# Kernel tuning notes

Hardware: AMD Instinct MI355X
Metric: run time of the kernel (lower is better)

## Reference

```python
import jax, jax.numpy as jnp
import numpy as np

B, L, E, H, V, ENC = 64, 51, 512, 512, 30000, 2048


def setup_inputs() -> dict:
    key = jax.random.key(0)
    ks = jax.random.split(key, 12)
    encoder_out = jax.random.normal(ks[0], (B, ENC), jnp.float32)
    encoded_captions = jax.random.randint(ks[1], (B, L), 0, V)
    lengths = jax.random.randint(ks[2], (B,), 2, L + 1)
    lengths = lengths.at[0].set(L)  # ensure max(decode_lengths) == L-1 so T is static
    caption_lengths = lengths[:, None]

    def lin(k, out_d, in_d):
        bnd = 1.0 / np.sqrt(in_d)
        kw, kb = jax.random.split(k)
        w = jax.random.uniform(kw, (out_d, in_d), jnp.float32, -bnd, bnd)
        b = jax.random.uniform(kb, (out_d,), jnp.float32, -bnd, bnd)
        return w, b

    embedding_weight = jax.random.uniform(ks[3], (V, E), jnp.float32, -0.1, 0.1)
    w_ih, b_ih = lin(ks[4], 4 * H, E)
    w_hh, b_hh = lin(ks[5], 4 * H, H)
    w_init_h, b_init_h = lin(ks[6], H, ENC)
    w_init_c, b_init_c = lin(ks[7], H, ENC)
    w_fc = jax.random.uniform(ks[8], (V, H), jnp.float32, -0.1, 0.1)
    b_fc = jnp.zeros((V,), jnp.float32)
    return dict(encoder_out=encoder_out, encoded_captions=encoded_captions,
                caption_lengths=caption_lengths, embedding_weight=embedding_weight,
                w_ih=w_ih, b_ih=b_ih, w_hh=w_hh, b_hh=b_hh,
                w_init_h=w_init_h, b_init_h=b_init_h,
                w_init_c=w_init_c, b_init_c=b_init_c, w_fc=w_fc, b_fc=b_fc)


def _forward(encoder_out, embedding_weight, w_ih, b_ih, w_hh, b_hh,
             w_init_h, b_init_h, w_init_c, b_init_c, w_fc, b_fc,
             encoded_captions, caption_lengths):
    lengths = caption_lengths[:, 0]
    sort_ind = jnp.argsort(-lengths)          # descending-length sort
    enc = encoder_out[sort_ind]
    caps = encoded_captions[sort_ind]
    dec_len = lengths[sort_ind] - 1           # [B]
    embs = embedding_weight[caps]             # [B, L, E]
    h0 = enc @ w_init_h.T + b_init_h          # [B, H]
    c0 = enc @ w_init_c.T + b_init_c
    T = caps.shape[1] - 1                     # static max(decode_lengths)
    xs = (jnp.transpose(embs[:, :T], (1, 0, 2)), jnp.arange(T))

    # Note: the torch loop trims h,c to batch_size_t; because lengths are
    # sorted descending, trimmed rows never produce outputs again, so running
    # the full batch and masking finished rows yields identical predictions.
    def step(carry, xt):
        h, c = carry
        x, t = xt
        gates = x @ w_ih.T + b_ih + h @ w_hh.T + b_hh   # [B, 4H]
        i, f, g, o = jnp.split(gates, 4, axis=-1)       # LSTMCell gate order
        c = jax.nn.sigmoid(f) * c + jax.nn.sigmoid(i) * jnp.tanh(g)
        h = jax.nn.sigmoid(o) * jnp.tanh(c)
        preds = h @ w_fc.T + b_fc                        # dropout = identity (eval)
        preds = jnp.where((t < dec_len)[:, None], preds, 0.0)
        return (h, c), preds

    _, preds = jax.lax.scan(step, (h0, c0), xs)          # [T, B, V]
    predictions = jnp.transpose(preds, (1, 0, 2))        # [B, T, V]
    return predictions, caps, dec_len, sort_ind


def reference(encoder_out, encoded_captions, caption_lengths, embedding_weight,
              w_ih, b_ih, w_hh, b_hh, w_init_h, b_init_h, w_init_c, b_init_c,
              w_fc, b_fc):
    return _forward(encoder_out, embedding_weight, w_ih, b_ih, w_hh, b_hh,
                    w_init_h, b_init_h, w_init_c, b_init_c, w_fc, b_fc,
                    encoded_captions, caption_lengths)
```

## Files before the change

kernel.cpp:

```cpp
#include <hip/hip_runtime.h>

#define NB    64
#define LCAP  51
#define TT    50
#define HID   512
#define EMB   512
#define VOC   30000
#define ENCD  2048
#define G4    2048

typedef unsigned short u16;
typedef unsigned int   u32;
typedef __attribute__((ext_vector_type(8))) short bf16x8;
typedef __attribute__((ext_vector_type(4))) float f32x4;
typedef __attribute__((ext_vector_type(4))) unsigned int u32x4;

__device__ __forceinline__ u16 f2bf(float x) {
  union { float f; unsigned u; } v; v.f = x;
  unsigned r = v.u + 0x7fffu + ((v.u >> 16) & 1u);
  return (u16)(r >> 16);
}

__device__ __forceinline__ float fast_sigmoid(float x) {
  return 1.f / (1.f + __expf(-x));
}
__device__ __forceinline__ float fast_tanh(float x) {
  float xx = fminf(fmaxf(x, -10.f), 10.f);
  float e = __expf(2.f * xx);
  return (e - 1.f) * __frcp_rn(e + 1.f);
}

template <int SLEEP>
__device__ __forceinline__ void poll_flags16(const int* flg, int lane, u32 tt) {
  if (lane < 16) {
    const u32* myp = (const u32*)flg + lane;
    u32 f;
    for (;;) {
      asm volatile("global_load_dword %0, %1, off sc0 sc1"
                   : "=v"(f) : "v"(myp) : "memory");
      asm volatile("s_waitcnt vmcnt(0)" : "+v"(f) :: "memory");
      if (((f & 0xffu) >= tt) & (((f >> 8) & 0xffu) >= tt) &
          (((f >> 16) & 0xffu) >= tt) & ((f >> 24) >= tt)) break;
      __builtin_amdgcn_s_sleep(SLEEP);
    }
  }
}

__global__ __launch_bounds__(256) void sort_k(const int* __restrict__ cap_len,
                                              const int* __restrict__ caps,
                                              float* __restrict__ out,
                                              int* __restrict__ sind,
                                              int* __restrict__ dlen,
                                              int* __restrict__ trow,
                                              int* __restrict__ zmap,
                                              int* __restrict__ nact,
                                              int* __restrict__ flags,
                                              int* __restrict__ tileneed) {
  __shared__ int smlen[NB];
  __shared__ int smpos[NB];
  __shared__ int sdl[NB];
  __shared__ int cnt_s[TT];
  __shared__ int toff_s[TT];
  __shared__ int trow_s[NB * TT];
  int tid = threadIdx.x;
  if (tid < NB) { smlen[tid] = cap_len[tid]; flags[tid] = 0; }
  __syncthreads();
  if (tid < NB) {
    int li = smlen[tid];
    int rank = 0;
    for (int j = 0; j < NB; ++j) {
      int lj = smlen[j];
      rank += (lj > li || (lj == li && j < tid)) ? 1 : 0;
    }
    smpos[rank] = tid;
  }
  __syncthreads();
  if (tid < NB) {
    int src = smpos[tid];
    int dl = smlen[src] - 1;
    sind[tid] = src;
    dlen[tid] = dl;
    sdl[tid] = dl;
    float* caps_out = out + (size_t)NB * TT * VOC;
    for (int l = 0; l < LCAP; ++l)
      caps_out[tid * LCAP + l] = (float)caps[src * LCAP + l];
    out[96003264 + tid] = (float)dl;
    out[96003328 + tid] = (float)src;
  }
  __syncthreads();
  if (tid < TT) {
    int c = 0;
    for (int b = 0; b < NB; ++b) c += (sdl[b] > tid) ? 1 : 0;
    cnt_s[tid] = c;
  }
  __syncthreads();
  if (tid == 0) {
    int s = 0;
    for (int t = 0; t < TT; ++t) { toff_s[t] = s; s += cnt_s[t]; }
    *nact = s;
  }
  __syncthreads();
  if (tid < TT) {
    int t = tid;
    int o = toff_s[t];
    int z = t * NB - o;
    int c = cnt_s[t];
    for (int b = 0; b < NB; ++b) {
      int m = b * TT + t;
      if (b < c) trow_s[o + b] = m;
      else       zmap[z + (b - c)] = m;
    }
  }
  __syncthreads();
  int na = toff_s[TT - 1] + cnt_s[TT - 1];
  for (int k = tid; k < na; k += 256) trow[k] = trow_s[k];
  if (tid < 25) {
    int i = tid;
    if (i * 128 < na) {
      int k = min(i * 128 + 127, na - 1);
      tileneed[i] = (trow_s[k] % TT) + 2;
    }
  }
}

__global__ __launch_bounds__(256) void conv4(const float* __restrict__ src,
                                             u16* __restrict__ dst, int n4) {
  int i = blockIdx.x * 256 + threadIdx.x;
  if (i >= n4) return;
  float4 v = ((const float4*)src)[i];
  ushort4 o;
  o.x = f2bf(v.x); o.y = f2bf(v.y); o.z = f2bf(v.z); o.w = f2bf(v.w);
  ((ushort4*)dst)[i] = o;
}

__global__ __launch_bounds__(256) void conv_winit_k(const float* __restrict__ wh,
                                                    const float* __restrict__ wc,
                                                    u16* __restrict__ dst) {
  int i = blockIdx.x * 256 + threadIdx.x;
  if (i >= 524288) return;
  int e = i * 4;
  int row = e >> 11;
  int col = e & 2047;
  const float* src = (row < 512) ? (wh + (size_t)row * 2048 + col)
                                 : (wc + (size_t)(row - 512) * 2048 + col);
  float4 v = *(const float4*)src;
  ushort4 o;
  o.x = f2bf(v.x); o.y = f2bf(v.y); o.z = f2bf(v.z); o.w = f2bf(v.w);
  ((ushort4*)dst)[i] = o;
}

__global__ __launch_bounds__(256) void gather_enc_k(const float* __restrict__ enc,
                                                    const int* __restrict__ sind,
                                                    u16* __restrict__ dst) {
  int i = blockIdx.x * 256 + threadIdx.x;
  if (i >= 32768) return;
  int e = i * 4;
  int r = e >> 11;
  int k = e & 2047;
  float4 v = *(const float4*)(enc + (size_t)sind[r] * ENCD + k);
  ushort4 o;
  o.x = f2bf(v.x); o.y = f2bf(v.y); o.z = f2bf(v.z); o.w = f2bf(v.w);
  ((ushort4*)dst)[i] = o;
}

__global__ __launch_bounds__(256) void gather_x_k(const float* __restrict__ emb,
                                                  const int* __restrict__ caps,
                                                  const int* __restrict__ sind,
                                                  u16* __restrict__ dst) {
  int i = blockIdx.x * 256 + threadIdx.x;
  if (i >= 409600) return;
  int e = i * 4;
  int m = e >> 9;
  int k = e & 511;
  unsigned b = ((unsigned)m * 5243u) >> 18;
  int t = m - (int)b * TT;
  int cap = caps[sind[b] * LCAP + t];
  float4 v = *(const float4*)(emb + (size_t)cap * EMB + k);
  ushort4 o;
  o.x = f2bf(v.x); o.y = f2bf(v.y); o.z = f2bf(v.z); o.w = f2bf(v.w);
  ((ushort4*)dst)[i] = o;
}

#define BM 128
#define BN 128
#define BK 32
#define LDT 40

template <int EPI>
__global__ __launch_bounds__(256) void gemm_bt(const u16* __restrict__ A,
                                               const u16* __restrict__ Bm,
                                               int Mr, int Nr, int K,
                                               void* __restrict__ outv,
                                               float* __restrict__ out1,
                                               const float* __restrict__ bias0,
                                               const float* __restrict__ bias1) {
  __shared__ u16 As[BM * LDT];
  __shared__ u16 Bs[BN * LDT];
  int tid = threadIdx.x;
  int mBase = blockIdx.x * BM;
  int nBase = blockIdx.y * BN;

  int wid = tid >> 6, lane = tid & 63;
  int wm = (wid >> 1) * 64, wn = (wid & 1) * 64;
  int lm = lane & 15, lq = lane >> 4;

  f32x4 acc[4][4];
  for (int i = 0; i < 4; ++i)
    for (int j = 0; j < 4; ++j)
      acc[i][j] = (f32x4){0.f, 0.f, 0.f, 0.f};

  int nkt = K / BK;
  for (int kt = 0; kt < nkt; ++kt) {
    for (int it = 0; it < 2; ++it) {
      int li = tid + it * 256;
      int row = li >> 2, kq = li & 3;
      {
        int gr = min(mBase + row, Mr - 1);
        uint4 v = *(const uint4*)(A + (size_t)gr * K + kt * BK + kq * 8);
        *(uint4*)&As[row * LDT + kq * 8] = v;
      }
      {
        int gr = min(nBase + row, Nr - 1);
        uint4 v = *(const uint4*)(Bm + (size_t)gr * K + kt * BK + kq * 8);
        *(uint4*)&Bs[row * LDT + kq * 8] = v;
      }
    }
    __syncthreads();
    bf16x8 af[4], bfr[4];
    for (int i = 0; i < 4; ++i)
      af[i] = *(const bf16x8*)&As[(wm + i * 16 + lm) * LDT + lq * 8];
    for (int j = 0; j < 4; ++j)
      bfr[j] = *(const bf16x8*)&Bs[(wn + j * 16 + lm) * LDT + lq * 8];
    for (int i = 0; i < 4; ++i)
      for (int j = 0; j < 4; ++j)
        acc[i][j] = __builtin_amdgcn_mfma_f32_16x16x32_bf16(af[i], bfr[j], acc[i][j], 0, 0, 0);
    __syncthreads();
  }

  for (int i = 0; i < 4; ++i) {
    int rloc0 = wm + i * 16 + (lane >> 4) * 4;
    for (int j = 0; j < 4; ++j) {
      int col = nBase + wn + j * 16 + (lane & 15);
      for (int r = 0; r < 4; ++r) {
        int rloc = rloc0 + r;
        float v = acc[i][j][r];
        if (EPI == 0) {
          int row = mBase + rloc;
          if (row < Mr && col < Nr)
            ((float*)outv)[(size_t)row * Nr + col] = v + bias0[col] + bias1[col];
        } else {
          int row = mBase + rloc;
          if (row < Mr && col < Nr) {
            if (col < 512) {
              int jj = col >> 3;
              ((u16*)outv)[(size_t)jj * 512 + row * 8 + (col & 7)] = f2bf(v + bias0[col]);
            } else {
              out1[(size_t)row * 512 + (col - 512)] = v + bias1[col - 512];
            }
          }
        }
      }
    }
  }
}

__global__ __launch_bounds__(256, 1) void lstm_fc(const float* __restrict__ w_hh,
                                                  const float* __restrict__ xW,
                                                  const float* __restrict__ cbuf,
                                                  u32* __restrict__ hx,
                                                  u32* __restrict__ Hs32,
                                                  int* __restrict__ flg,
                                                  const u16* __restrict__ Wfc,
                                                  const float* __restrict__ b_fc,
                                                  const int* __restrict__ trow,
                                                  const int* __restrict__ zmap,
                                                  const int* __restrict__ nactp,
                                                  const int* __restrict__ tileneed,
                                                  float* __restrict__ out) {
  __shared__ __align__(16) char smem[43520];
  int tid = threadIdx.x;
  int wave = tid >> 6, lane = tid & 63;
  int lm = lane & 15, lq = lane >> 4;

  if (blockIdx.x < 64) {
    u16* wsm = (u16*)smem;
    float* gsmf = (float*)(smem + 33280);
    u32* hsh = (u32*)(smem + 33280 + 9216);
#define GSM(rr, cc) gsmf[(rr) * 36 + (cc)]
    int j = blockIdx.x;
    int u0 = j * 8;

    {
      int r = tid >> 3;
      int cc = (tid & 7) * 64;
      const float* src = w_hh + (size_t)((r >> 3) * HID + u0 + (r & 7)) * HID + cc;
      u16* dst = &wsm[r * 520 + cc];
#pragma unroll
      for (int q = 0; q < 16; ++q) {
        float4 v = ((const float4*)src)[q];
        ushort4 o; o.x = f2bf(v.x); o.y = f2bf(v.y); o.z = f2bf(v.z); o.w = f2bf(v.w);
        ((ushort4*)dst)[q] = o;
      }
    }
    __syncthreads();

    bf16x8 bfrag[2][16];
#pragma unroll
    for (int n = 0; n < 2; ++n)
#pragma unroll
      for (int kq = 0; kq < 16; ++kq)
        bfrag[n][kq] = *(const bf16x8*)&wsm[(n * 16 + lm) * 520 + kq * 32 + lq * 8];

    int b = tid >> 2, up = tid & 3;
    float creg[2];
    {
      float2 c2 = *(const float2*)&cbuf[(size_t)b * HID + u0 + 2 * up];
      creg[0] = c2.x; creg[1] = c2.y;
    }

    const int abase = lq * 256 + (wave * 16 + lm) * 4;

    for (int t = 0; t < TT; ++t) {
      const u32* hcur = hx + (size_t)(t & 1) * (NB * 256);
      u32* hnxt = hx + (size_t)((t + 1) & 1) * (NB * 256);

      float xg[4][2];
      {
        const float* xwp = xW + (size_t)(b * TT + t) * G4 + u0 + 2 * up;
#pragma unroll
        for (int g = 0; g < 4; ++g) {
          float2 v = *(const float2*)&xwp[g * HID];
          xg[g][0] = v.x; xg[g][1] = v.y;
        }
      }

      if (t > 0) {
        if (wave == 0) poll_flags16<1>(flg, lane, (u32)t);
        __syncthreads();
      }

      u32x4 raw[16];
#pragma unroll
      for (int kq = 0; kq < 16; ++kq) {
        const u32* p = hcur + abase + kq * 1024;
        asm volatile("global_load_dwordx4 %0, %1, off sc0 sc1"
                     : "=v"(raw[kq]) : "v"(p) : "memory");
      }
      asm volatile("s_waitcnt vmcnt(0)"
                   : "+v"(raw[0]), "+v"(raw[1]), "+v"(raw[2]), "+v"(raw[3]),
                     "+v"(raw[4]), "+v"(raw[5]), "+v"(raw[6]), "+v"(raw[7]),
                     "+v"(raw[8]), "+v"(raw[9]), "+v"(raw[10]), "+v"(raw[11]),
                     "+v"(raw[12]), "+v"(raw[13]), "+v"(raw[14]), "+v"(raw[15])
                   :: "memory");

      f32x4 acc0 = (f32x4){0.f, 0.f, 0.f, 0.f};
      f32x4 acc1 = (f32x4){0.f, 0.f, 0.f, 0.f};
#pragma unroll
      for (int kq = 0; kq < 16; ++kq) {
        bf16x8 a = __builtin_bit_cast(bf16x8, raw[kq]);
        acc0 = __builtin_amdgcn_mfma_f32_16x16x32_bf16(a, bfrag[0][kq], acc0, 0, 0, 0);
        acc1 = __builtin_amdgcn_mfma_f32_16x16x32_bf16(a, bfrag[1][kq], acc1, 0, 0, 0);
      }
#pragma unroll
      for (int r = 0; r < 4; ++r) {
        GSM(wave * 16 + lq * 4 + r, lm)      = acc0[r];
        GSM(wave * 16 + lq * 4 + r, 16 + lm) = acc1[r];
      }

      float hn2[2];
#pragma unroll
      for (int e = 0; e < 2; ++e) {
        int ul = 2 * up + e;
        float gi = GSM(b, ul)      + xg[0][e];
        float gf = GSM(b, 8 + ul)  + xg[1][e];
        float gg = GSM(b, 16 + ul) + xg[2][e];
        float go = GSM(b, 24 + ul) + xg[3][e];
        float cn = fast_sigmoid(gf) * creg[e] + fast_sigmoid(gi) * fast_tanh(gg);
        creg[e] = cn;
        hn2[e] = fast_sigmoid(go) * fast_tanh(cn);
      }
      hsh[b * 4 + up] = (u32)f2bf(hn2[0]) | ((u32)f2bf(hn2[1]) << 16);
      __syncthreads();

      if (tid < 64) {
        u32x4 hv = *(const u32x4*)&hsh[tid * 4];
        u32* dst = hnxt + j * 256 + tid * 4;
        asm volatile("global_store_dwordx4 %0, %1, off sc0 sc1"
                     :: "v"(dst), "v"(hv) : "memory");
        asm volatile("s_waitcnt vmcnt(0)" ::: "memory");
        if (tid == 0) {
          u32 fv = (u32)(t + 1);
          unsigned char* fj = (unsigned char*)flg + j;
          asm volatile("global_store_byte %0, %1, off sc0 sc1"
                       :: "v"(fj), "v"(fv) : "memory");
        }
        u32* hdst = Hs32 + ((size_t)tid * TT + t) * 256 + j * 4;
        asm volatile("global_store_dwordx4 %0, %1, off sc0 sc1"
                     :: "v"(hdst), "v"(hv) : "memory");
      }
    }
    if (wave == 0) {
      asm volatile("s_waitcnt vmcnt(0)" ::: "memory");
      if (lane == 0) {
        u32 fv = 51u;
        unsigned char* fj = (unsigned char*)flg + j;
        asm volatile("global_store_byte %0, %1, off sc0 sc1"
                     :: "v"(fj), "v"(fv) : "memory");
      }
    }
#undef GSM
  } else {
    u16* As = (u16*)smem;
    u16* Bs = (u16*)(smem + 10240);
    int* rmap_s = (int*)(smem + 20480);
    int* tn_s = (int*)(smem + 20992);
    const u16* HsA = (const u16*)Hs32;

    if (tid < 25) tn_s[tid] = tileneed[tid];
    int nactv = nactp[0];
    int ntiles = (nactv + 127) >> 7;
    int totjobs = ntiles * 235;
    __syncthreads();

    const int F = 192;
    int f = blockIdx.x - 64;
    int wm = (wave >> 1) * 64, wn = (wave & 1) * 64;

    int lastNeed = 0;
    for (int job = f; job < totjobs; job += F) {
      int rt = job / 235;
      int nb = job - rt * 235;
      int nBase = nb * 128;
      int need = tn_s[rt];
      if (need > lastNeed) {
        if (wave == 0) poll_flags16<64>(flg, lane, (u32)need);
        lastNeed = need;
      }
      __syncthreads();
      if (tid < 128) {
        int k = (rt << 7) + tid;
        rmap_s[tid] = trow[(k < nactv) ? k : (nactv - 1)];
      }
      __syncthreads();

      f32x4 acc[4][4];
      for (int i = 0; i < 4; ++i)
        for (int jj = 0; jj < 4; ++jj)
          acc[i][jj] = (f32x4){0.f, 0.f, 0.f, 0.f};

      for (int kt = 0; kt < 16; ++kt) {
        for (int it = 0; it < 2; ++it) {
          int li = tid + it * 256;
          int row = li >> 2, kq = li & 3;
          {
            int gr = rmap_s[row];
            uint4 v = *(const uint4*)(HsA + (size_t)gr * 512 + kt * BK + kq * 8);
            *(uint4*)&As[row * LDT + kq * 8] = v;
          }
          {
            int gb = min(nBase + row, VOC - 1);
            uint4 v = *(const uint4*)(Wfc + (size_t)gb * 512 + kt * BK + kq * 8);
            *(uint4*)&Bs[row * LDT + kq * 8] = v;
          }
        }
        __syncthreads();
        bf16x8 af[4], bfr[4];
        for (int i = 0; i < 4; ++i)
          af[i] = *(const bf16x8*)&As[(wm + i * 16 + lm) * LDT + lq * 8];
        for (int jj = 0; jj < 4; ++jj)
          bfr[jj] = *(const bf16x8*)&Bs[(wn + jj * 16 + lm) * LDT + lq * 8];
        for (int i = 0; i < 4; ++i)
          for (int jj = 0; jj < 4; ++jj)
            acc[i][jj] = __builtin_amdgcn_mfma_f32_16x16x32_bf16(af[i], bfr[jj], acc[i][jj], 0, 0, 0);
        __syncthreads();
      }

      for (int i = 0; i < 4; ++i) {
        int rloc0 = wm + i * 16 + lq * 4;
        for (int jj = 0; jj < 4; ++jj) {
          int col = nBase + wn + jj * 16 + lm;
          if (col < VOC) {
            float bias = b_fc[col];
            for (int r = 0; r < 4; ++r) {
              int m = rmap_s[rloc0 + r];
              out[(size_t)m * VOC + col] = acc[i][jj][r] + bias;
            }
          }
        }
      }
    }

    int nz = NB * TT - nactv;
    float4 zz = {0.f, 0.f, 0.f, 0.f};
    for (int r = f; r < nz; r += F) {
      float4* dst = (float4*)(out + (size_t)zmap[r] * VOC);
      for (int c4 = tid; c4 < VOC / 4; c4 += 256) dst[c4] = zz;
    }
  }
}

extern "C" void kernel_launch(void* const* d_in, const int* in_sizes, int n_in,
                              void* d_out, int out_size, void* d_ws, size_t ws_size,
                              hipStream_t stream) {
  const float* encoder_out = (const float*)d_in[0];
  const int*   caps        = (const int*)d_in[1];
  const int*   cap_len     = (const int*)d_in[2];
  const float* emb         = (const float*)d_in[3];
  const float* w_ih        = (const float*)d_in[4];
  const float* b_ih        = (const float*)d_in[5];
  const float* w_hh        = (const float*)d_in[6];
  const float* b_hh        = (const float*)d_in[7];
  const float* w_init_h    = (const float*)d_in[8];
  const float* b_init_h    = (const float*)d_in[9];
  const float* w_init_c    = (const float*)d_in[10];
  const float* b_init_c    = (const float*)d_in[11];
  const float* w_fc        = (const float*)d_in[12];
  const float* b_fc        = (const float*)d_in[13];
  float* out = (float*)d_out;

  char* ws = (char*)d_ws;
  int*   sind    = (int*)(ws + 0);
  int*   dlen    = (int*)(ws + 256);
  int*   nact    = (int*)(ws + 512);
  int*   flags   = (int*)(ws + 576);
  int*   tilend  = (int*)(ws + 640);
  int*   trow    = (int*)(ws + 832);
  int*   zmap    = (int*)(ws + 13632);
  float* cbuf    = (float*)(ws + 26496);
  u16*   hbuf    = (u16*)(ws + 157568);
  float* xW      = (float*)(ws + 288640);
  u16*   Hs      = (u16*)(ws + 26503040);
  u16*   Xb      = (u16*)(ws + 29779840);
  u16*   Wih     = (u16*)(ws + 33056640);
  u16*   Winit   = (u16*)(ws + 35153792);
  u16*   Wfc     = (u16*)(ws + 39348096);
  u16*   Ebf     = (u16*)(ws + 70068096);

  sort_k<<<1, 256, 0, stream>>>(cap_len, caps, out, sind, dlen, trow, zmap,
                                nact, flags, tilend);
  conv4<<<1024, 256, 0, stream>>>(w_ih, Wih, 262144);
  conv_winit_k<<<2048, 256, 0, stream>>>(w_init_h, w_init_c, Winit);
  conv4<<<15000, 256, 0, stream>>>(w_fc, Wfc, 3840000);
  gather_enc_k<<<128, 256, 0, stream>>>(encoder_out, sind, Ebf);
  gather_x_k<<<1600, 256, 0, stream>>>(emb, caps, sind, Xb);

  gemm_bt<1><<<dim3(1, 8), 256, 0, stream>>>(Ebf, Winit, 64, 1024, 2048,
                                             hbuf, cbuf, b_init_h, b_init_c);
  gemm_bt<0><<<dim3(25, 16), 256, 0, stream>>>(Xb, Wih, 3200, 2048, 512,
                                               xW, nullptr, b_ih, b_hh);
  lstm_fc<<<256, 256, 0, stream>>>(w_hh, xW, cbuf, (u32*)hbuf, (u32*)Hs, flags,
                                   Wfc, b_fc, trow, zmap, nact, tilend, out);
}
```

Measured before the change: 866.9 us.

## Fuse prep kernels and convert FC weights inside the persistent LSTM kernel

Merges the four small conversion and gather kernels into one prep launch to cut launch overhead. The large w_fc fp32-to-bf16 conversion moves into the FC worker blocks of the persistent LSTM kernel, so it overlaps with the recurrent blocks instead of running as a separate pass beforehand. FC jobs are now split into contiguous vocabulary-column ranges per block, so each block converts only its own columns, and are iterated row-tile-major to fit that ownership. The risks are load imbalance, more redundant loads of the A tile across columns, and reliance on each block reading only the Wfc rows it converted itself.

Result: no change. 859.8 us (-0.8%).

```diff
diff --git a/kernel.cpp b/kernel.cpp
--- a/kernel.cpp
+++ b/kernel.cpp
@@ -123,62 +123,47 @@
   }
 }
 
-__global__ __launch_bounds__(256) void conv4(const float* __restrict__ src,
-                                             u16* __restrict__ dst, int n4) {
+__global__ __launch_bounds__(256) void prep_k(const float* __restrict__ w_ih,
+                                              const float* __restrict__ wh,
+                                              const float* __restrict__ wc,
+                                              const float* __restrict__ enc,
+                                              const float* __restrict__ emb,
+                                              const int* __restrict__ caps,
+                                              const int* __restrict__ sind,
+                                              u16* __restrict__ Wih,
+                                              u16* __restrict__ Winit,
+                                              u16* __restrict__ Ebf,
+                                              u16* __restrict__ Xb) {
   int i = blockIdx.x * 256 + threadIdx.x;
-  if (i >= n4) return;
-  float4 v = ((const float4*)src)[i];
-  ushort4 o;
-  o.x = f2bf(v.x); o.y = f2bf(v.y); o.z = f2bf(v.z); o.w = f2bf(v.w);
-  ((ushort4*)dst)[i] = o;
-}
-
-__global__ __launch_bounds__(256) void conv_winit_k(const float* __restrict__ wh,
-                                                    const float* __restrict__ wc,
-                                                    u16* __restrict__ dst) {
-  int i = blockIdx.x * 256 + threadIdx.x;
-  if (i >= 524288) return;
-  int e = i * 4;
-  int row = e >> 11;
-  int col = e & 2047;
-  const float* src = (row < 512) ? (wh + (size_t)row * 2048 + col)
-                                 : (wc + (size_t)(row - 512) * 2048 + col);
+  const float* src;
+  u16* dstp;
+  if (i < 262144) {
+    src = w_ih + (size_t)i * 4;
+    dstp = Wih + (size_t)i * 4;
+  } else if (i < 786432) {
+    int e = (i - 262144) * 4;
+    int row = e >> 11, col = e & 2047;
+    src = (row < 512) ? (wh + (size_t)row * 2048 + col)
+                      : (wc + (size_t)(row - 512) * 2048 + col);
+    dstp = Winit + (size_t)(i - 262144) * 4;
+  } else if (i < 819200) {
+    int e = (i - 786432) * 4;
+    int r = e >> 11, k = e & 2047;
+    src = enc + (size_t)sind[r] * ENCD + k;
+    dstp = Ebf + (size_t)(i - 786432) * 4;
+  } else if (i < 1228800) {
+    int e = (i - 819200) * 4;
+    int m = e >> 9, k = e & 511;
+    unsigned b = ((unsigned)m * 5243u) >> 18;
+    int t = m - (int)b * TT;
+    int cap = caps[sind[b] * LCAP + t];
+    src = emb + (size_t)cap * EMB + k;
+    dstp = Xb + (size_t)(i - 819200) * 4;
+  } else return;
   float4 v = *(const float4*)src;
   ushort4 o;
   o.x = f2bf(v.x); o.y = f2bf(v.y); o.z = f2bf(v.z); o.w = f2bf(v.w);
-  ((ushort4*)dst)[i] = o;
-}
-
-__global__ __launch_bounds__(256) void gather_enc_k(const float* __restrict__ enc,
-                                                    const int* __restrict__ sind,
-                                                    u16* __restrict__ dst) {
-  int i = blockIdx.x * 256 + threadIdx.x;
-  if (i >= 32768) return;
-  int e = i * 4;
-  int r = e >> 11;
-  int k = e & 2047;
-  float4 v = *(const float4*)(enc + (size_t)sind[r] * ENCD + k);
-  ushort4 o;
-  o.x = f2bf(v.x); o.y = f2bf(v.y); o.z = f2bf(v.z); o.w = f2bf(v.w);
-  ((ushort4*)dst)[i] = o;
-}
-
-__global__ __launch_bounds__(256) void gather_x_k(const float* __restrict__ emb,
-                                                  const int* __restrict__ caps,
-                                                  const int* __restrict__ sind,
-                                                  u16* __restrict__ dst) {
-  int i = blockIdx.x * 256 + threadIdx.x;
-  if (i >= 409600) return;
-  int e = i * 4;
-  int m = e >> 9;
-  int k = e & 511;
-  unsigned b = ((unsigned)m * 5243u) >> 18;
-  int t = m - (int)b * TT;
-  int cap = caps[sind[b] * LCAP + t];
-  float4 v = *(const float4*)(emb + (size_t)cap * EMB + k);
-  ushort4 o;
-  o.x = f2bf(v.x); o.y = f2bf(v.y); o.z = f2bf(v.z); o.w = f2bf(v.w);
-  ((ushort4*)dst)[i] = o;
+  *(ushort4*)dstp = o;
 }
 
 #define BM 128
@@ -270,7 +255,8 @@
                                                   u32* __restrict__ hx,
                                                   u32* __restrict__ Hs32,
                                                   int* __restrict__ flg,
-                                                  const u16* __restrict__ Wfc,
+                                                  const float* __restrict__ w_fc,
+                                                  u16* __restrict__ Wfc,
                                                   const float* __restrict__ b_fc,
                                                   const int* __restrict__ trow,
                                                   const int* __restrict__ zmap,
@@ -424,66 +410,98 @@
 
     const int F = 192;
     int f = blockIdx.x - 64;
+    int fs = (f & 7) * 24 + (f >> 3);
+    int per = (totjobs + F - 1) / F;
+    int J0 = fs * per;
+    int J1 = min(J0 + per, totjobs);
     int wm = (wave >> 1) * 64, wn = (wave & 1) * 64;
 
-    int lastNeed = 0;
-    for (int job = f; job < totjobs; job += F) {
-      int rt = job / 235;
-      int nb = job - rt * 235;
-      int nBase = nb * 128;
-      int need = tn_s[rt];
-      if (need > lastNeed) {
-        if (wave == 0) poll_flags16<64>(flg, lane, (u32)need);
-        lastNeed = need;
+    if (J0 < J1) {
+      int p0 = J0 / ntiles, p1 = (J1 - 1) / ntiles;
+
+      for (int p = p0; p <= p1; ++p) {
+        int r0 = p * 128;
+        int r1 = min(r0 + 128, VOC);
+        int nel4 = (r1 - r0) * 128;
+        const float4* src = (const float4*)(w_fc + (size_t)r0 * 512);
+        ushort4* dst = (ushort4*)(Wfc + (size_t)r0 * 512);
+        for (int i = tid; i < nel4; i += 256) {
+          float4 v = src[i];
+          ushort4 o;
+          o.x = f2bf(v.x); o.y = f2bf(v.y); o.z = f2bf(v.z); o.w = f2bf(v.w);
+          dst[i] = o;
+        }
       }
       __syncthreads();
-      if (tid < 128) {
-        int k = (rt << 7) + tid;
-        rmap_s[tid] = trow[(k < nactv) ? k : (nactv - 1)];
-      }
-      __syncthreads();
-
-      f32x4 acc[4][4];
-      for (int i = 0; i < 4; ++i)
-        for (int jj = 0; jj < 4; ++jj)
-          acc[i][jj] = (f32x4){0.f, 0.f, 0.f, 0.f};
-
-      for (int kt = 0; kt < 16; ++kt) {
-        for (int it = 0; it < 2; ++it) {
-          int li = tid + it * 256;
-          int row = li >> 2, kq = li & 3;
-          {
-            int gr = rmap_s[row];
-            uint4 v = *(const uint4*)(HsA + (size_t)gr * 512 + kt * BK + kq * 8);
-            *(uint4*)&As[row * LDT + kq * 8] = v;
+
+      int lastNeed = 0;
+      for (int rt = 0; rt < ntiles; ++rt) {
+        int need = tn_s[rt];
+        bool any = false;
+        for (int p = p0; p <= p1; ++p) {
+          int J = p * ntiles + rt;
+          if (J >= J0 && J < J1) { any = true; break; }
+        }
+        if (!any) continue;
+        if (need > lastNeed) {
+          if (wave == 0) poll_flags16<64>(flg, lane, (u32)need);
+          lastNeed = need;
+        }
+        __syncthreads();
+        if (tid < 128) {
+          int k = (rt << 7) + tid;
+          rmap_s[tid] = trow[(k < nactv) ? k : (nactv - 1)];
+        }
+        __syncthreads();
+
+        for (int p = p0; p <= p1; ++p) {
+          int J = p * ntiles + rt;
+          if (J < J0 || J >= J1) continue;
+          int nBase = p * 128;
+
+          f32x4 acc[4][4];
+          for (int i = 0; i < 4; ++i)
+            for (int jj = 0; jj < 4; ++jj)
+              acc[i][jj] = (f32x4){0.f, 0.f, 0.f, 0.f};
+
+          for (int kt = 0; kt < 16; ++kt) {
+            for (int it = 0; it < 2; ++it) {
+              int li = tid + it * 256;
+              int row = li >> 2, kq = li & 3;
+              {
+                int gr = rmap_s[row];
+                uint4 v = *(const uint4*)(HsA + (size_t)gr * 512 + kt * BK + kq * 8);
+                *(uint4*)&As[row * LDT + kq * 8] = v;
+              }
+              {
+                int gb = min(nBase + row, VOC - 1);
+                uint4 v = *(const uint4*)(Wfc + (size_t)gb * 512 + kt * BK + kq * 8);
+                *(uint4*)&Bs[row * LDT + kq * 8] = v;
+              }
+            }
+            __syncthreads();
+            bf16x8 af[4], bfr[4];
+            for (int i = 0; i < 4; ++i)
+              af[i] = *(const bf16x8*)&As[(wm + i * 16 + lm) * LDT + lq * 8];
+            for (int jj = 0; jj < 4; ++jj)
+              bfr[jj] = *(const bf16x8*)&Bs[(wn + jj * 16 + lm) * LDT + lq * 8];
+            for (int i = 0; i < 4; ++i)
+              for (int jj = 0; jj < 4; ++jj)
+                acc[i][jj] = __builtin_amdgcn_mfma_f32_16x16x32_bf16(af[i], bfr[jj], acc[i][jj], 0, 0, 0);
+            __syncthreads();
           }
-          {
-            int gb = min(nBase + row, VOC - 1);
-            uint4 v = *(const uint4*)(Wfc + (size_t)gb * 512 + kt * BK + kq * 8);
-            *(uint4*)&Bs[row * LDT + kq * 8] = v;
-          }
-        }
-        __syncthreads();
-        bf16x8 af[4], bfr[4];
-        for (int i = 0; i < 4; ++i)
-          af[i] = *(const bf16x8*)&As[(wm + i * 16 + lm) * LDT + lq * 8];
-        for (int jj = 0; jj < 4; ++jj)
-          bfr[jj] = *(const bf16x8*)&Bs[(wn + jj * 16 + lm) * LDT + lq * 8];
-        for (int i = 0; i < 4; ++i)
-          for (int jj = 0; jj < 4; ++jj)
-            acc[i][jj] = __builtin_amdgcn_mfma_f32_16x16x32_bf16(af[i], bfr[jj], acc[i][jj], 0, 0, 0);
-        __syncthreads();
-      }
-
-      for (int i = 0; i < 4; ++i) {
-        int rloc0 = wm + i * 16 + lq * 4;
-        for (int jj = 0; jj < 4; ++jj) {
-          int col = nBase + wn + jj * 16 + lm;
-          if (col < VOC) {
-            float bias = b_fc[col];
-            for (int r = 0; r < 4; ++r) {
-              int m = rmap_s[rloc0 + r];
-              out[(size_t)m * VOC + col] = acc[i][jj][r] + bias;
+
+          for (int i = 0; i < 4; ++i) {
+            int rloc0 = wm + i * 16 + lq * 4;
+            for (int jj = 0; jj < 4; ++jj) {
+              int col = nBase + wn + jj * 16 + lm;
+              if (col < VOC) {
+                float bias = b_fc[col];
+                for (int r = 0; r < 4; ++r) {
+                  int m = rmap_s[rloc0 + r];
+                  out[(size_t)m * VOC + col] = acc[i][jj][r] + bias;
+                }
+              }
             }
           }
         }
@@ -538,16 +556,13 @@
 
   sort_k<<<1, 256, 0, stream>>>(cap_len, caps, out, sind, dlen, trow, zmap,
                                 nact, flags, tilend);
-  conv4<<<1024, 256, 0, stream>>>(w_ih, Wih, 262144);
-  conv_winit_k<<<2048, 256, 0, stream>>>(w_init_h, w_init_c, Winit);
-  conv4<<<15000, 256, 0, stream>>>(w_fc, Wfc, 3840000);
-  gather_enc_k<<<128, 256, 0, stream>>>(encoder_out, sind, Ebf);
-  gather_x_k<<<1600, 256, 0, stream>>>(emb, caps, sind, Xb);
+  prep_k<<<4800, 256, 0, stream>>>(w_ih, w_init_h, w_init_c, encoder_out,
+                                   emb, caps, sind, Wih, Winit, Ebf, Xb);
 
   gemm_bt<1><<<dim3(1, 8), 256, 0, stream>>>(Ebf, Winit, 64, 1024, 2048,
                                              hbuf, cbuf, b_init_h, b_init_c);
   gemm_bt<0><<<dim3(25, 16), 256, 0, stream>>>(Xb, Wih, 3200, 2048, 512,
                                                xW, nullptr, b_ih, b_hh);
   lstm_fc<<<256, 256, 0, stream>>>(w_hh, xW, cbuf, (u32*)hbuf, (u32*)Hs, flags,
-                                   Wfc, b_fc, trow, zmap, nact, tilend, out);
-}
+                                   w_fc, Wfc, b_fc, trow, zmap, nact, tilend, out);
+}
```
